# Kernel optimization log

Measured on AMD Instinct MI355X. Metric: run time of the kernel, lower is better.

The kernel has to match this reference:

```python
import jax, jax.numpy as jnp
import numpy as np

T, D, E, K = 16384, 2048, 128, 8

def setup_inputs() -> dict:
    key = jax.random.key(0)
    k1, k2 = jax.random.split(key)
    hidden_states = jax.random.normal(k1, (T, D), dtype=jnp.float32)
    weight = jax.random.normal(k2, (E, D), dtype=jnp.float32) * 0.02
    return {"hidden_states": hidden_states, "weight": weight}

def reference(hidden_states, weight):
    # (T, D) @ (D, E) -> (T, E) router logits
    x = hidden_states.reshape(-1, weight.shape[1])
    logits = jnp.einsum('td,ed->te', x, weight)
    # softmax in float32 over experts
    router_logits = jax.nn.softmax(logits.astype(jnp.float32), axis=-1)
    # top-k selection + renormalization so selected weights sum to 1
    router_weights, router_indices = jax.lax.top_k(router_logits, K)
    router_weights = router_weights / jnp.sum(router_weights, axis=-1, keepdims=True)
    return (router_logits, router_weights, router_indices)
```

## Files before the change

kernel.cpp:

```cpp
#include <hip/hip_runtime.h>
#include <math.h>


constexpr int T = 16384;
constexpr int D = 2048;
constexpr int E = 128;
constexpr int K = 8;

constexpr int BM  = 32;
constexpr int NS  = 5;
constexpr int NB2 = D / 128;

typedef int i32x4 __attribute__((ext_vector_type(4)));

#define MFI8(A, B, C) C = __builtin_amdgcn_mfma_i32_16x16x64_i8(A, B, C, 0, 0, 0)

__device__ __forceinline__ void slice5(float x, float c, float ic, int out[NS]) {
    float r = x;
#pragma unroll
    for (int s = 0; s < NS; ++s) {
        float q = rintf(r * c);
        out[s] = (int)q;
        r = fmaf(q, -ic, r);
        c *= 128.f;
        ic *= (1.f / 128.f);
    }
}

__global__ __launch_bounds__(256)
void w_slice(const float* __restrict__ W, signed char* __restrict__ Ws)
{
    const int e  = blockIdx.x >> 1;
    const int k0 = ((blockIdx.x & 1) << 10) | (threadIdx.x << 2);
    float4 v = *(const float4*)(W + (size_t)e * D + k0);
    int b0[NS], b1[NS], b2[NS], b3[NS];
    slice5(v.x, 512.f, 1.f / 512.f, b0);
    slice5(v.y, 512.f, 1.f / 512.f, b1);
    slice5(v.z, 512.f, 1.f / 512.f, b2);
    slice5(v.w, 512.f, 1.f / 512.f, b3);
#pragma unroll
    for (int s = 0; s < NS; ++s) {
        unsigned lo = __builtin_amdgcn_perm((unsigned)b1[s], (unsigned)b0[s], 0x00000400u);
        unsigned hi = __builtin_amdgcn_perm((unsigned)b3[s], (unsigned)b2[s], 0x00000400u);
        unsigned pk = __builtin_amdgcn_perm(hi, lo, 0x05040100u);
        *(int*)(Ws + (size_t)s * E * D + (size_t)e * D + k0) = (int)pk;
    }
}

__global__ __launch_bounds__(512, 4)
void router_fused(const float* __restrict__ X,
                  const signed char* __restrict__ Ws,
                  float* __restrict__ out)
{
    __shared__ __align__(16) signed char As[2][2][NS][2][4][16][16];
    __shared__ double Ld[BM][E];

    const int tid = threadIdx.x;
    const long t0 = (long)blockIdx.x * BM;

    const int ar = tid >> 4;
    const int ac = (tid & 15) << 2;
    const float* Xp = X + (t0 + ar) * (long)D + ac;

    const int l  = tid & 63;
    const int wv = tid >> 6;
    const int er = l & 15;
    const int kg = l >> 4;

    const size_t wbase = (size_t)(wv * 16 + er) * D + (size_t)kg * 16;
    const signed char* Wq0 = Ws + 0UL * E * D + wbase;
    const signed char* Wq1 = Ws + 1UL * E * D + wbase;
    const signed char* Wq2 = Ws + 2UL * E * D + wbase;
    const signed char* Wq3 = Ws + 3UL * E * D + wbase;
    const signed char* Wq4 = Ws + 4UL * E * D + wbase;

    const int loff = kg * 256 + (((er + (kg << 2)) & 15) << 4);

    i32x4 e0 = {}, e1 = {}, e2 = {}, e3 = {}, e4 = {};
    i32x4 f0 = {}, f1 = {}, f2 = {}, f3 = {}, f4 = {};

    auto stage = [&](const float4& v, int buf, int chn) {
        int q0[NS], q1[NS], q2[NS], q3[NS];
        slice5(v.x, 16.f, 1.f / 16.f, q0);
        slice5(v.y, 16.f, 1.f / 16.f, q1);
        slice5(v.z, 16.f, 1.f / 16.f, q2);
        slice5(v.w, 16.f, 1.f / 16.f, q3);
        const int slot = ((ar & 15) + ((ac >> 4) << 2)) & 15;
        int* dst = (int*)&As[buf][chn][0][ar >> 4][ac >> 4][slot][ac & 15];
#pragma unroll
        for (int s = 0; s < NS; ++s) {
            unsigned lo = __builtin_amdgcn_perm((unsigned)q1[s], (unsigned)q0[s], 0x00000400u);
            unsigned hi = __builtin_amdgcn_perm((unsigned)q3[s], (unsigned)q2[s], 0x00000400u);
            unsigned pk = __builtin_amdgcn_perm(hi, lo, 0x05040100u);
            dst[s * 512] = (int)pk;
        }
    };

    auto chunkMM = [&](const signed char* ap,
                       const i32x4& b0, const i32x4& b1, const i32x4& b2,
                       const i32x4& b3, const i32x4& b4) {
        i32x4 at0, at1;
        at0 = *(const i32x4*)(ap);           at1 = *(const i32x4*)(ap + 1024);
        MFI8(at0, b0, e0); MFI8(at0, b1, e1); MFI8(at0, b2, e2); MFI8(at0, b3, e3); MFI8(at0, b4, e4);
        MFI8(at1, b0, f0); MFI8(at1, b1, f1); MFI8(at1, b2, f2); MFI8(at1, b3, f3); MFI8(at1, b4, f4);
        at0 = *(const i32x4*)(ap + 2048);    at1 = *(const i32x4*)(ap + 3072);
        MFI8(at0, b0, e1); MFI8(at0, b1, e2); MFI8(at0, b2, e3); MFI8(at0, b3, e4);
        MFI8(at1, b0, f1); MFI8(at1, b1, f2); MFI8(at1, b2, f3); MFI8(at1, b3, f4);
        at0 = *(const i32x4*)(ap + 4096);    at1 = *(const i32x4*)(ap + 5120);
        MFI8(at0, b0, e2); MFI8(at0, b1, e3); MFI8(at0, b2, e4);
        MFI8(at1, b0, f2); MFI8(at1, b1, f3); MFI8(at1, b2, f4);
        at0 = *(const i32x4*)(ap + 6144);    at1 = *(const i32x4*)(ap + 7168);
        MFI8(at0, b0, e3); MFI8(at0, b1, e4);
        MFI8(at1, b0, f3); MFI8(at1, b1, f4);
        at0 = *(const i32x4*)(ap + 8192);    at1 = *(const i32x4*)(ap + 9216);
        MFI8(at0, b0, e4);
        MFI8(at1, b0, f4);
    };

    float4 xv0, xv1;
    {
        float4 x0 = *(const float4*)(Xp);
        float4 x1 = *(const float4*)(Xp + 64);
        stage(x0, 0, 0);
        stage(x1, 0, 1);
        xv0 = *(const float4*)(Xp + 128);
        xv1 = *(const float4*)(Xp + 192);
        __syncthreads();
    }

    for (int p = 0; p < NB2; ++p) {
        const int cur = p & 1;
        const long kb = (long)p * 128;

        i32x4 b00 = *(const i32x4*)(Wq0 + kb);
        i32x4 b01 = *(const i32x4*)(Wq1 + kb);
        i32x4 b02 = *(const i32x4*)(Wq2 + kb);
        i32x4 b03 = *(const i32x4*)(Wq3 + kb);
        i32x4 b04 = *(const i32x4*)(Wq4 + kb);
        i32x4 b10 = *(const i32x4*)(Wq0 + kb + 64);
        i32x4 b11 = *(const i32x4*)(Wq1 + kb + 64);
        i32x4 b12 = *(const i32x4*)(Wq2 + kb + 64);
        i32x4 b13 = *(const i32x4*)(Wq3 + kb + 64);
        i32x4 b14 = *(const i32x4*)(Wq4 + kb + 64);

        if (p < NB2 - 1) {
            stage(xv0, cur ^ 1, 0);
            stage(xv1, cur ^ 1, 1);
        }
        if (p < NB2 - 2) {
            xv0 = *(const float4*)(Xp + (p + 2) * 128);
            xv1 = *(const float4*)(Xp + (p + 2) * 128 + 64);
        }

        const signed char* ap =
            (const signed char*)&As[cur][0][0][0][0][0][0] + loff;
        chunkMM(ap,         b00, b01, b02, b03, b04);
        chunkMM(ap + 10240, b10, b11, b12, b13, b14);

        __syncthreads();
    }

#pragma unroll
    for (int r = 0; r < 4; ++r) {
        const int row = kg * 4 + r;
        const int col = wv * 16 + er;
        Ld[row][col]      = (double)e0[r] * 0x1p-13 + (double)e1[r] * 0x1p-20
                          + (double)e2[r] * 0x1p-27 + (double)e3[r] * 0x1p-34
                          + (double)e4[r] * 0x1p-41;
        Ld[row + 16][col] = (double)f0[r] * 0x1p-13 + (double)f1[r] * 0x1p-20
                          + (double)f2[r] * 0x1p-27 + (double)f3[r] * 0x1p-34
                          + (double)f4[r] * 0x1p-41;
    }
    __syncthreads();

    float* outL  = out;
    float* outWt = out + (long)T * E;
    float* outId = outWt + (long)T * K;
    const int tx = tid & 15;
    const int tt = tid >> 4;
    const long t = t0 + tt;

    double acc[8];
#pragma unroll
    for (int j = 0; j < 8; ++j) acc[j] = Ld[tt][(tx << 3) + j];

    double m = acc[0];
#pragma unroll
    for (int j = 1; j < 8; ++j) m = fmax(m, acc[j]);
#pragma unroll
    for (int mask = 1; mask <= 8; mask <<= 1)
        m = fmax(m, __shfl_xor(m, mask, 64));

    float e[8]; float s = 0.f;
#pragma unroll
    for (int j = 0; j < 8; ++j) { e[j] = __expf((float)(acc[j] - m)); s += e[j]; }
#pragma unroll
    for (int mask = 1; mask <= 8; mask <<= 1)
        s += __shfl_xor(s, mask, 64);
    const float inv = 1.f / s;

    float4 st0 = {e[0] * inv, e[1] * inv, e[2] * inv, e[3] * inv};
    float4 st1 = {e[4] * inv, e[5] * inv, e[6] * inv, e[7] * inv};
    *(float4*)&outL[t * E + (tx << 3)]     = st0;
    *(float4*)&outL[t * E + (tx << 3) + 4] = st1;

    double v[8];
#pragma unroll
    for (int j = 0; j < 8; ++j) v[j] = acc[j];

    float pk[K]; int ik[K]; float tsum = 0.f;
#pragma unroll
    for (int r = 0; r < K; ++r) {
        double bv = -1.0e300; int bi = 0x7fffffff;
#pragma unroll
        for (int j = 0; j < 8; ++j) {
            const int idx = (tx << 3) + j;
            const bool better = (v[j] > bv) || (v[j] == bv && idx < bi);
            bv = better ? v[j] : bv;
            bi = better ? idx : bi;
        }
#pragma unroll
        for (int mask = 1; mask <= 8; mask <<= 1) {
            const double ov = __shfl_xor(bv, mask, 64);
            const int    oi = __shfl_xor(bi, mask, 64);
            const bool better = (ov > bv) || (ov == bv && oi < bi);
            bv = better ? ov : bv;
            bi = better ? oi : bi;
        }
        const float pw = __expf((float)(bv - m)) * inv;
        pk[r] = pw; ik[r] = bi; tsum += pw;
        const bool own  = ((bi >> 3) == tx);
        const int  slot = bi & 7;
#pragma unroll
        for (int j = 0; j < 8; ++j)
            v[j] = (own && j == slot) ? -1.0e300 : v[j];
    }

    if (tx == 0) {
        const float rinv = 1.f / tsum;
#pragma unroll
        for (int r = 0; r < K; ++r) {
            outWt[t * K + r] = pk[r] * rinv;
            outId[t * K + r] = (float)ik[r];
        }
    }
}

extern "C" void kernel_launch(void* const* d_in, const int* in_sizes, int n_in,
                              void* d_out, int out_size, void* d_ws, size_t ws_size,
                              hipStream_t stream)
{
    const float* X = (const float*)d_in[0];
    const float* W = (const float*)d_in[1];
    float* out = (float*)d_out;
    signed char* Ws = (signed char*)d_ws;

    w_slice<<<dim3(E * 2), dim3(256), 0, stream>>>(W, Ws);
    router_fused<<<dim3(T / BM), dim3(512), 0, stream>>>(X, Ws, out);
}
```

Baseline: 252.6 us.

## Split router into expert-half GEMM blocks plus separate softmax/top-k kernel

```diff
diff --git a/kernel.cpp b/kernel.cpp
--- a/kernel.cpp
+++ b/kernel.cpp
@@ -47,27 +47,28 @@
     }
 }
 
-__global__ __launch_bounds__(512, 4)
-void router_fused(const float* __restrict__ X,
-                  const signed char* __restrict__ Ws,
-                  float* __restrict__ out)
+__global__ __launch_bounds__(256, 4)
+void router_gemm(const float* __restrict__ X,
+                 const signed char* __restrict__ Ws,
+                 double* __restrict__ wsd)
 {
     __shared__ __align__(16) signed char As[2][2][NS][2][4][16][16];
-    __shared__ double Ld[BM][E];
 
     const int tid = threadIdx.x;
-    const long t0 = (long)blockIdx.x * BM;
-
-    const int ar = tid >> 4;
-    const int ac = (tid & 15) << 2;
-    const float* Xp = X + (t0 + ar) * (long)D + ac;
+    const int bx  = blockIdx.x;
+    const long t0 = (long)(bx >> 1) * BM;
+    const int eh  = (bx & 1) << 6;
+
+    const int ar = tid >> 3;
+    const int ak = tid & 7;
+    const float* Xp = X + (t0 + ar) * (long)D + (ak << 2);
 
     const int l  = tid & 63;
     const int wv = tid >> 6;
     const int er = l & 15;
     const int kg = l >> 4;
 
-    const size_t wbase = (size_t)(wv * 16 + er) * D + (size_t)kg * 16;
+    const size_t wbase = (size_t)(eh + wv * 16 + er) * D + (size_t)kg * 16;
     const signed char* Wq0 = Ws + 0UL * E * D + wbase;
     const signed char* Wq1 = Ws + 1UL * E * D + wbase;
     const signed char* Wq2 = Ws + 2UL * E * D + wbase;
@@ -79,14 +80,16 @@
     i32x4 e0 = {}, e1 = {}, e2 = {}, e3 = {}, e4 = {};
     i32x4 f0 = {}, f1 = {}, f2 = {}, f3 = {}, f4 = {};
 
-    auto stage = [&](const float4& v, int buf, int chn) {
+    auto stage = [&](const float4& v, int buf, int c) {
         int q0[NS], q1[NS], q2[NS], q3[NS];
         slice5(v.x, 16.f, 1.f / 16.f, q0);
         slice5(v.y, 16.f, 1.f / 16.f, q1);
         slice5(v.z, 16.f, 1.f / 16.f, q2);
         slice5(v.w, 16.f, 1.f / 16.f, q3);
-        const int slot = ((ar & 15) + ((ac >> 4) << 2)) & 15;
-        int* dst = (int*)&As[buf][chn][0][ar >> 4][ac >> 4][slot][ac & 15];
+        const int chn  = c >> 1;
+        const int kgv  = (ak >> 2) + ((c & 1) << 1);
+        const int slot = ((ar & 15) + (kgv << 2)) & 15;
+        int* dst = (int*)&As[buf][chn][0][ar >> 4][kgv][slot][(ak & 3) << 2];
 #pragma unroll
         for (int s = 0; s < NS; ++s) {
             unsigned lo = __builtin_amdgcn_perm((unsigned)q1[s], (unsigned)q0[s], 0x00000400u);
@@ -117,16 +120,16 @@
         MFI8(at1, b0, f4);
     };
 
-    float4 xv0, xv1;
-    {
-        float4 x0 = *(const float4*)(Xp);
-        float4 x1 = *(const float4*)(Xp + 64);
-        stage(x0, 0, 0);
-        stage(x1, 0, 1);
-        xv0 = *(const float4*)(Xp + 128);
-        xv1 = *(const float4*)(Xp + 192);
-        __syncthreads();
-    }
+    float4 xv0 = *(const float4*)(Xp);
+    float4 xv1 = *(const float4*)(Xp + 32);
+    float4 xv2 = *(const float4*)(Xp + 64);
+    float4 xv3 = *(const float4*)(Xp + 96);
+    stage(xv0, 0, 0); stage(xv1, 0, 1); stage(xv2, 0, 2); stage(xv3, 0, 3);
+    xv0 = *(const float4*)(Xp + 128);
+    xv1 = *(const float4*)(Xp + 160);
+    xv2 = *(const float4*)(Xp + 192);
+    xv3 = *(const float4*)(Xp + 224);
+    __syncthreads();
 
     for (int p = 0; p < NB2; ++p) {
         const int cur = p & 1;
@@ -137,24 +140,32 @@
         i32x4 b02 = *(const i32x4*)(Wq2 + kb);
         i32x4 b03 = *(const i32x4*)(Wq3 + kb);
         i32x4 b04 = *(const i32x4*)(Wq4 + kb);
+
+        if (p < NB2 - 1) {
+            stage(xv0, cur ^ 1, 0);
+            stage(xv1, cur ^ 1, 1);
+            stage(xv2, cur ^ 1, 2);
+            stage(xv3, cur ^ 1, 3);
+        }
+
         i32x4 b10 = *(const i32x4*)(Wq0 + kb + 64);
         i32x4 b11 = *(const i32x4*)(Wq1 + kb + 64);
         i32x4 b12 = *(const i32x4*)(Wq2 + kb + 64);
         i32x4 b13 = *(const i32x4*)(Wq3 + kb + 64);
         i32x4 b14 = *(const i32x4*)(Wq4 + kb + 64);
 
-        if (p < NB2 - 1) {
-            stage(xv0, cur ^ 1, 0);
-            stage(xv1, cur ^ 1, 1);
-        }
-        if (p < NB2 - 2) {
-            xv0 = *(const float4*)(Xp + (p + 2) * 128);
-            xv1 = *(const float4*)(Xp + (p + 2) * 128 + 64);
-        }
-
         const signed char* ap =
             (const signed char*)&As[cur][0][0][0][0][0][0] + loff;
-        chunkMM(ap,         b00, b01, b02, b03, b04);
+        chunkMM(ap, b00, b01, b02, b03, b04);
+
+        if (p < NB2 - 2) {
+            const long kn = (long)(p + 2) * 128;
+            xv0 = *(const float4*)(Xp + kn);
+            xv1 = *(const float4*)(Xp + kn + 32);
+            xv2 = *(const float4*)(Xp + kn + 64);
+            xv3 = *(const float4*)(Xp + kn + 96);
+        }
+
         chunkMM(ap + 10240, b10, b11, b12, b13, b14);
 
         __syncthreads();
@@ -163,26 +174,38 @@
 #pragma unroll
     for (int r = 0; r < 4; ++r) {
         const int row = kg * 4 + r;
-        const int col = wv * 16 + er;
-        Ld[row][col]      = (double)e0[r] * 0x1p-13 + (double)e1[r] * 0x1p-20
-                          + (double)e2[r] * 0x1p-27 + (double)e3[r] * 0x1p-34
-                          + (double)e4[r] * 0x1p-41;
-        Ld[row + 16][col] = (double)f0[r] * 0x1p-13 + (double)f1[r] * 0x1p-20
-                          + (double)f2[r] * 0x1p-27 + (double)f3[r] * 0x1p-34
-                          + (double)f4[r] * 0x1p-41;
-    }
-    __syncthreads();
+        const int col = eh + wv * 16 + er;
+        wsd[(t0 + row) * E + col]      = (double)e0[r] * 0x1p-13 + (double)e1[r] * 0x1p-20
+                                       + (double)e2[r] * 0x1p-27 + (double)e3[r] * 0x1p-34
+                                       + (double)e4[r] * 0x1p-41;
+        wsd[(t0 + row + 16) * E + col] = (double)f0[r] * 0x1p-13 + (double)f1[r] * 0x1p-20
+                                       + (double)f2[r] * 0x1p-27 + (double)f3[r] * 0x1p-34
+                                       + (double)f4[r] * 0x1p-41;
+    }
+}
+
+__global__ __launch_bounds__(256)
+void router_top(const double* __restrict__ wsd, float* __restrict__ out)
+{
+    const int tid = threadIdx.x;
+    const int tx  = tid & 15;
+    const int tt  = tid >> 4;
+    const long t  = (long)blockIdx.x * 16 + tt;
 
     float* outL  = out;
     float* outWt = out + (long)T * E;
     float* outId = outWt + (long)T * K;
-    const int tx = tid & 15;
-    const int tt = tid >> 4;
-    const long t = t0 + tt;
 
     double acc[8];
-#pragma unroll
-    for (int j = 0; j < 8; ++j) acc[j] = Ld[tt][(tx << 3) + j];
+    {
+        const double* s = wsd + t * E + (tx << 3);
+#pragma unroll
+        for (int h = 0; h < 4; ++h) {
+            double2 u = *(const double2*)(s + 2 * h);
+            acc[2 * h + 0] = u.x;
+            acc[2 * h + 1] = u.y;
+        }
+    }
 
     double m = acc[0];
 #pragma unroll
@@ -253,8 +276,11 @@
     const float* X = (const float*)d_in[0];
     const float* W = (const float*)d_in[1];
     float* out = (float*)d_out;
-    signed char* Ws = (signed char*)d_ws;
+
+    double* wsd = (double*)d_ws;
+    signed char* Ws = (signed char*)d_ws + (size_t)T * E * sizeof(double);
 
     w_slice<<<dim3(E * 2), dim3(256), 0, stream>>>(W, Ws);
-    router_fused<<<dim3(T / BM), dim3(512), 0, stream>>>(X, Ws, out);
-}
+    router_gemm<<<dim3(2 * (T / BM)), dim3(256), 0, stream>>>(X, Ws, wsd);
+    router_top<<<dim3(T / 16), dim3(256), 0, stream>>>(wsd, out);
+}
```

New measurement: 265.7 us. 1.05x slower.
